# Optimization experiments

Hardware: AMD Instinct MI355X
Metric: run time of the kernel (lower is better)

## Reference

```python
import jax, jax.numpy as jnp
import numpy as np

E = 512
H = 8
D = E // H  # 64
B = 2
S = 4096


def setup_inputs() -> dict:
    key = jax.random.key(0)
    ks = jax.random.split(key, 12)
    s = 1.0 / np.sqrt(E)
    return {
        "x": jax.random.normal(ks[0], (B, S, E), dtype=jnp.float32),
        "bias": jax.random.normal(ks[1], (H, 1, S, S), dtype=jnp.float32),
        "mask": jax.random.randint(ks[2], (1, 1, S, S), 0, 2, dtype=jnp.int32),
        "Wq": jax.random.normal(ks[3], (E, E), dtype=jnp.float32) * s,
        "bq": jnp.zeros((E,), dtype=jnp.float32),
        "Wk": jax.random.normal(ks[4], (E, E), dtype=jnp.float32) * s,
        "bk": jnp.zeros((E,), dtype=jnp.float32),
        "Wv": jax.random.normal(ks[5], (E, E), dtype=jnp.float32) * s,
        "bv": jnp.zeros((E,), dtype=jnp.float32),
        "Wo": jax.random.normal(ks[6], (E, E), dtype=jnp.float32) * s,
        "bo": jnp.zeros((E,), dtype=jnp.float32),
    }


def _split_heads(t):
    # [B,S,E] -> [H,B,S,D]  (matches x.view(B,-1,H,D).permute(2,0,1,3))
    b, s, _ = t.shape
    return t.reshape(b, s, H, D).transpose(2, 0, 1, 3)


def reference(x, bias, mask, Wq, bq, Wk, bk, Wv, bv, Wo, bo):
    # torch Linear: y = x @ W.T + b
    q = _split_heads(x @ Wq.T + bq)  # [H,B,S,D]
    k = _split_heads(x @ Wk.T + bk)
    v = _split_heads(x @ Wv.T + bv)

    scores = jnp.einsum("hbqd,hbkd->hbqk", q, k) + bias  # [H,B,S,S]
    scores = jnp.where(mask == 0, jnp.float32(-1e20), scores)
    # NOTE: original divides AFTER bias-add and masking
    probs = jax.nn.softmax(scores / jnp.sqrt(jnp.float32(D)), axis=-1)
    out = jnp.einsum("hbqk,hbkd->hbqd", probs, v)  # [H,B,S,D]
    out = out.transpose(1, 2, 0, 3).reshape(x.shape[0], -1, H * D)  # [B,S,E]
    return out @ Wo.T + bo
```

## Files before the change

### kernel.cpp

```cpp
#include <hip/hip_runtime.h>
#include <hip/hip_bf16.h>

typedef __bf16 bf16x8 __attribute__((ext_vector_type(8)));
typedef float f32x4 __attribute__((ext_vector_type(4)));

#define S_LEN 4096
#define EMB   512
#define NHEAD 8
#define HDIM  64
#define NBAT  2
#define NROW  (NBAT * S_LEN)

static __device__ __forceinline__ f32x4 mfma16x16(bf16x8 a, bf16x8 b, f32x4 c) {
    return __builtin_amdgcn_mfma_f32_16x16x32_bf16(a, b, c, 0, 0, 0);
}

__global__ __launch_bounds__(256) void convert_kernel(
    const float* __restrict__ x, const float* __restrict__ Wq,
    const float* __restrict__ Wk, const float* __restrict__ Wv,
    const float* __restrict__ Wo,
    __hip_bfloat16* __restrict__ xb, __hip_bfloat16* __restrict__ wqkv,
    __hip_bfloat16* __restrict__ wob)
{
    const int NX = NROW * EMB;
    const int NW = EMB * EMB;
    int i = blockIdx.x * 256 + threadIdx.x;
    if (i < NX) { xb[i] = __float2bfloat16(x[i]); return; }
    int j = i - NX;
    if (j < 3 * NW) {
        int p = j >> 18, r = j & (NW - 1);
        const float* src = (p == 0) ? Wq : (p == 1) ? Wk : Wv;
        wqkv[j] = __float2bfloat16(src[r]);
    } else if (j < 4 * NW) {
        int r = j - 3 * NW;
        wob[r] = __float2bfloat16(Wo[r]);
    }
}

__device__ __forceinline__ void gemm_core(
    const __hip_bfloat16* __restrict__ A, const __hip_bfloat16* __restrict__ Bw,
    int mbase, int nbase,
    __hip_bfloat16* As, __hip_bfloat16* Bs, f32x4 acc[2][4])
{
    const int tid = threadIdx.x;
    const int w = tid >> 6, lane = tid & 63, l = lane & 15, quad = lane >> 4;
    const f32x4 zero = {0.f, 0.f, 0.f, 0.f};
#pragma unroll
    for (int mb = 0; mb < 2; mb++)
#pragma unroll
        for (int nb = 0; nb < 4; nb++) acc[mb][nb] = zero;

    for (int k0 = 0; k0 < EMB; k0 += 32) {
        __syncthreads();
#pragma unroll
        for (int c = tid; c < 512; c += 256) {
            int row = c >> 2, kc = c & 3;
            uint4 v = *(const uint4*)(A + (size_t)(mbase + row) * EMB + k0 + kc * 8);
            *(uint4*)(As + row * 40 + kc * 8) = v;
        }
        {
            int row = tid >> 2, kc = tid & 3;
            uint4 v = *(const uint4*)(Bw + (size_t)(nbase + row) * EMB + k0 + kc * 8);
            *(uint4*)(Bs + row * 40 + kc * 8) = v;
        }
        __syncthreads();

        bf16x8 af[2], bfr[4];
#pragma unroll
        for (int mb = 0; mb < 2; mb++)
            af[mb] = *(const bf16x8*)(As + (w * 32 + mb * 16 + l) * 40 + quad * 8);
#pragma unroll
        for (int nb = 0; nb < 4; nb++)
            bfr[nb] = *(const bf16x8*)(Bs + (nb * 16 + l) * 40 + quad * 8);
#pragma unroll
        for (int mb = 0; mb < 2; mb++)
#pragma unroll
            for (int nb = 0; nb < 4; nb++)
                acc[mb][nb] = mfma16x16(af[mb], bfr[nb], acc[mb][nb]);
    }
}

__global__ __launch_bounds__(256, 4) void qkv_gemm(
    const __hip_bfloat16* __restrict__ xb, const __hip_bfloat16* __restrict__ wqkv,
    const float* __restrict__ bq, const float* __restrict__ bk, const float* __restrict__ bv,
    __hip_bfloat16* __restrict__ Qh, __hip_bfloat16* __restrict__ Kh,
    __hip_bfloat16* __restrict__ Vt)
{
    __shared__ __align__(16) __hip_bfloat16 As[128 * 40];
    __shared__ __align__(16) __hip_bfloat16 Bs[64 * 40];
    const int mbase = blockIdx.x * 128, nbase = blockIdx.y * 64;
    f32x4 acc[2][4];
    gemm_core(xb, wqkv, mbase, nbase, As, Bs, acc);

    const int tid = threadIdx.x;
    const int w = tid >> 6, lane = tid & 63, l = lane & 15, quad = lane >> 4;
    const int p = nbase >> 9;
    const float* bias = (p == 0) ? bq : (p == 1) ? bk : bv;
    __hip_bfloat16* dst = (p == 0) ? Qh : (p == 1) ? Kh : Vt;
#pragma unroll
    for (int mb = 0; mb < 2; mb++)
#pragma unroll
        for (int nb = 0; nb < 4; nb++)
#pragma unroll
            for (int r = 0; r < 4; r++) {
                int m = mbase + w * 32 + mb * 16 + quad * 4 + r;
                int n = nbase + nb * 16 + l;
                int o = n & 511;
                float v = acc[mb][nb][r] + bias[o];
                int b = m >> 12, s = m & 4095, hh = o >> 6, d = o & 63;
                size_t idx = (p == 2)
                    ? ((size_t)((hh * 2 + b) * 64 + d)) * 4096 + s
                    : ((size_t)((hh * 2 + b) * 4096 + s)) * 64 + d;
                dst[idx] = __float2bfloat16(v);
            }
}

__global__ __launch_bounds__(256, 2) void attn_kernel(
    const __hip_bfloat16* __restrict__ Qh, const __hip_bfloat16* __restrict__ Kh,
    const __hip_bfloat16* __restrict__ Vt,
    const float* __restrict__ bias, const int* __restrict__ mask,
    __hip_bfloat16* __restrict__ Om)
{
    const int h = blockIdx.y, qt = blockIdx.x;
    const int tid = threadIdx.x;
    const int w = tid >> 6, lane = tid & 63, l = lane & 15, quad = lane >> 4;
    const int q0 = qt * 64;
    const float CS = 0.18033688011112042f;

    __shared__ __align__(16) __hip_bfloat16 Ks[2][64 * 72];
    __shared__ __align__(16) __hip_bfloat16 Vs[2][64 * 72];
    __shared__ __align__(16) __hip_bfloat16 Ps[64 * 72];

    bf16x8 qf[2][2];
#pragma unroll
    for (int b = 0; b < 2; b++) {
        const __hip_bfloat16* qp =
            Qh + ((size_t)((h * 2 + b) * 4096 + q0 + w * 16 + l)) * 64;
        qf[b][0] = *(const bf16x8*)(qp + quad * 8);
        qf[b][1] = *(const bf16x8*)(qp + 32 + quad * 8);
    }

    f32x4 oacc[2][4];
    float mst[2][4], lst[2][4];
    const f32x4 zero = {0.f, 0.f, 0.f, 0.f};
#pragma unroll
    for (int b = 0; b < 2; b++) {
#pragma unroll
        for (int nb = 0; nb < 4; nb++) oacc[b][nb] = zero;
#pragma unroll
        for (int r = 0; r < 4; r++) { mst[b][r] = -__builtin_inff(); lst[b][r] = 0.f; }
    }

    for (int kt = 0; kt < 64; kt++) {
        const int k0 = kt * 64;
        __syncthreads();
#pragma unroll
        for (int c = tid; c < 2048; c += 256) {
            int t = c >> 9;
            int b = t & 1, isV = t >> 1;
            int cc = c & 511, row = cc >> 3, ch = cc & 7;
            const __hip_bfloat16* src = isV
                ? Vt + ((size_t)((h * 2 + b) * 64 + row)) * 4096 + k0 + ch * 8
                : Kh + ((size_t)((h * 2 + b) * 4096 + k0 + row)) * 64 + ch * 8;
            uint4 v = *(const uint4*)src;
            *(uint4*)((isV ? Vs[b] : Ks[b]) + row * 72 + ch * 8) = v;
        }
        float bor[4][4];
#pragma unroll
        for (int nb = 0; nb < 4; nb++)
#pragma unroll
            for (int r = 0; r < 4; r++) {
                int qq = q0 + w * 16 + quad * 4 + r;
                int kk = k0 + nb * 16 + l;
                float bb = bias[(size_t)h * S_LEN * S_LEN + (size_t)qq * S_LEN + kk];
                int mm = mask[(size_t)qq * S_LEN + kk];
                bor[nb][r] = mm ? bb : -1e30f;
            }
        __syncthreads();

#pragma unroll
        for (int b = 0; b < 2; b++) {
            f32x4 sc[4] = {zero, zero, zero, zero};
#pragma unroll
            for (int ks = 0; ks < 2; ks++)
#pragma unroll
                for (int nb = 0; nb < 4; nb++) {
                    bf16x8 kf = *(const bf16x8*)(Ks[b] + (nb * 16 + l) * 72 + ks * 32 + quad * 8);
                    sc[nb] = mfma16x16(qf[b][ks], kf, sc[nb]);
                }
            float xv[4][4], rmax[4];
#pragma unroll
            for (int r = 0; r < 4; r++) rmax[r] = -__builtin_inff();
#pragma unroll
            for (int nb = 0; nb < 4; nb++)
#pragma unroll
                for (int r = 0; r < 4; r++) {
                    xv[nb][r] = (sc[nb][r] + bor[nb][r]) * CS;
                    rmax[r] = fmaxf(rmax[r], xv[nb][r]);
                }
#pragma unroll
            for (int r = 0; r < 4; r++) {
                rmax[r] = fmaxf(rmax[r], __shfl_xor(rmax[r], 1));
                rmax[r] = fmaxf(rmax[r], __shfl_xor(rmax[r], 2));
                rmax[r] = fmaxf(rmax[r], __shfl_xor(rmax[r], 4));
                rmax[r] = fmaxf(rmax[r], __shfl_xor(rmax[r], 8));
            }
            float alpha[4], rsum[4];
#pragma unroll
            for (int r = 0; r < 4; r++) {
                float mn = fmaxf(mst[b][r], rmax[r]);
                alpha[r] = __builtin_amdgcn_exp2f(mst[b][r] - mn);
                mst[b][r] = mn;
                rsum[r] = 0.f;
            }
            float pv[4][4];
#pragma unroll
            for (int nb = 0; nb < 4; nb++)
#pragma unroll
                for (int r = 0; r < 4; r++) {
                    float e = __builtin_amdgcn_exp2f(xv[nb][r] - mst[b][r]);
                    pv[nb][r] = e;
                    rsum[r] += e;
                }
#pragma unroll
            for (int r = 0; r < 4; r++) {
                rsum[r] += __shfl_xor(rsum[r], 1);
                rsum[r] += __shfl_xor(rsum[r], 2);
                rsum[r] += __shfl_xor(rsum[r], 4);
                rsum[r] += __shfl_xor(rsum[r], 8);
                lst[b][r] = lst[b][r] * alpha[r] + rsum[r];
            }
#pragma unroll
            for (int nb = 0; nb < 4; nb++)
#pragma unroll
                for (int r = 0; r < 4; r++) oacc[b][nb][r] *= alpha[r];
#pragma unroll
            for (int nb = 0; nb < 4; nb++)
#pragma unroll
                for (int r = 0; r < 4; r++)
                    Ps[(w * 16 + quad * 4 + r) * 72 + nb * 16 + l] =
                        __float2bfloat16(pv[nb][r]);
#pragma unroll
            for (int ks = 0; ks < 2; ks++) {
                bf16x8 pf = *(const bf16x8*)(Ps + (w * 16 + l) * 72 + ks * 32 + quad * 8);
#pragma unroll
                for (int nb = 0; nb < 4; nb++) {
                    bf16x8 vf = *(const bf16x8*)(Vs[b] + (nb * 16 + l) * 72 + ks * 32 + quad * 8);
                    oacc[b][nb] = mfma16x16(pf, vf, oacc[b][nb]);
                }
            }
        }
    }

#pragma unroll
    for (int b = 0; b < 2; b++)
#pragma unroll
        for (int nb = 0; nb < 4; nb++)
#pragma unroll
            for (int r = 0; r < 4; r++) {
                int qq = q0 + w * 16 + quad * 4 + r;
                float val = oacc[b][nb][r] / lst[b][r];
                Om[((size_t)(b * 4096 + qq)) * 512 + h * 64 + nb * 16 + l] =
                    __float2bfloat16(val);
            }
}

__global__ __launch_bounds__(256, 4) void out_gemm(
    const __hip_bfloat16* __restrict__ Om, const __hip_bfloat16* __restrict__ wob,
    const float* __restrict__ bo, float* __restrict__ out)
{
    __shared__ __align__(16) __hip_bfloat16 As[128 * 40];
    __shared__ __align__(16) __hip_bfloat16 Bs[64 * 40];
    const int mbase = blockIdx.x * 128, nbase = blockIdx.y * 64;
    f32x4 acc[2][4];
    gemm_core(Om, wob, mbase, nbase, As, Bs, acc);

    const int tid = threadIdx.x;
    const int w = tid >> 6, lane = tid & 63, l = lane & 15, quad = lane >> 4;
#pragma unroll
    for (int mb = 0; mb < 2; mb++)
#pragma unroll
        for (int nb = 0; nb < 4; nb++)
#pragma unroll
            for (int r = 0; r < 4; r++) {
                int m = mbase + w * 32 + mb * 16 + quad * 4 + r;
                int n = nbase + nb * 16 + l;
                out[(size_t)m * EMB + n] = acc[mb][nb][r] + bo[n];
            }
}

extern "C" void kernel_launch(void* const* d_in, const int* in_sizes, int n_in,
                              void* d_out, int out_size, void* d_ws, size_t ws_size,
                              hipStream_t stream) {
    const float* x    = (const float*)d_in[0];
    const float* bias = (const float*)d_in[1];
    const int*   mask = (const int*)d_in[2];
    const float* Wq   = (const float*)d_in[3];
    const float* bq   = (const float*)d_in[4];
    const float* Wk   = (const float*)d_in[5];
    const float* bk   = (const float*)d_in[6];
    const float* Wv   = (const float*)d_in[7];
    const float* bv   = (const float*)d_in[8];
    const float* Wo   = (const float*)d_in[9];
    const float* bo   = (const float*)d_in[10];
    float* out = (float*)d_out;

    char* ws = (char*)d_ws;
    __hip_bfloat16* xb   = (__hip_bfloat16*)ws; ws += (size_t)NROW * EMB * 2;
    __hip_bfloat16* wqkv = (__hip_bfloat16*)ws; ws += (size_t)3 * EMB * EMB * 2;
    __hip_bfloat16* wob  = (__hip_bfloat16*)ws; ws += (size_t)EMB * EMB * 2;
    __hip_bfloat16* Qh   = (__hip_bfloat16*)ws; ws += (size_t)NROW * EMB * 2;
    __hip_bfloat16* Kh   = (__hip_bfloat16*)ws; ws += (size_t)NROW * EMB * 2;
    __hip_bfloat16* Vt   = (__hip_bfloat16*)ws; ws += (size_t)NROW * EMB * 2;
    __hip_bfloat16* Om   = (__hip_bfloat16*)ws; ws += (size_t)NROW * EMB * 2;

    convert_kernel<<<dim3(20480), dim3(256), 0, stream>>>(
        x, Wq, Wk, Wv, Wo, xb, wqkv, wob);
    qkv_gemm<<<dim3(64, 24), dim3(256), 0, stream>>>(
        xb, wqkv, bq, bk, bv, Qh, Kh, Vt);
    attn_kernel<<<dim3(64, NHEAD), dim3(256), 0, stream>>>(
        Qh, Kh, Vt, bias, mask, Om);
    out_gemm<<<dim3(64, 8), dim3(256), 0, stream>>>(Om, wob, bo, out);
}
```

Baseline: 1.321 ms.

## Prefetch K/V and bias/mask into registers, split batches across waves, add V transpose kernel

The attention kernel now prefetches the next tile's K/V, bias and mask into registers while computing the current tile. Each wave handles one batch instead of both, so each block covers 32 queries and the grid doubles to 128x8 with a higher occupancy hint. The V transpose moves out of scattered qkv_gemm stores into a separate LDS-based transpose kernel that reuses the xb buffer. The aim is to hide global-load latency and improve store coalescing, at the cost of more registers per thread, one extra launch, and loading each K/V tile for half as many queries.

```diff
diff --git a/kernel.cpp b/kernel.cpp
--- a/kernel.cpp
+++ b/kernel.cpp
@@ -84,7 +84,7 @@
     const __hip_bfloat16* __restrict__ xb, const __hip_bfloat16* __restrict__ wqkv,
     const float* __restrict__ bq, const float* __restrict__ bk, const float* __restrict__ bv,
     __hip_bfloat16* __restrict__ Qh, __hip_bfloat16* __restrict__ Kh,
-    __hip_bfloat16* __restrict__ Vt)
+    __hip_bfloat16* __restrict__ Vh)
 {
     __shared__ __align__(16) __hip_bfloat16 As[128 * 40];
     __shared__ __align__(16) __hip_bfloat16 Bs[64 * 40];
@@ -96,7 +96,7 @@
     const int w = tid >> 6, lane = tid & 63, l = lane & 15, quad = lane >> 4;
     const int p = nbase >> 9;
     const float* bias = (p == 0) ? bq : (p == 1) ? bk : bv;
-    __hip_bfloat16* dst = (p == 0) ? Qh : (p == 1) ? Kh : Vt;
+    __hip_bfloat16* dst = (p == 0) ? Qh : (p == 1) ? Kh : Vh;
 #pragma unroll
     for (int mb = 0; mb < 2; mb++)
 #pragma unroll
@@ -108,14 +108,35 @@
                 int o = n & 511;
                 float v = acc[mb][nb][r] + bias[o];
                 int b = m >> 12, s = m & 4095, hh = o >> 6, d = o & 63;
-                size_t idx = (p == 2)
-                    ? ((size_t)((hh * 2 + b) * 64 + d)) * 4096 + s
-                    : ((size_t)((hh * 2 + b) * 4096 + s)) * 64 + d;
-                dst[idx] = __float2bfloat16(v);
-            }
-}
-
-__global__ __launch_bounds__(256, 2) void attn_kernel(
+                dst[((size_t)((hh * 2 + b) * 4096 + s)) * 64 + d] = __float2bfloat16(v);
+            }
+}
+
+__global__ __launch_bounds__(256) void vtrans(
+    const __hip_bfloat16* __restrict__ Vh, __hip_bfloat16* __restrict__ Vt)
+{
+    __shared__ __align__(16) __hip_bfloat16 T[64 * 72];
+    const int st = blockIdx.x, hb = blockIdx.y, tid = threadIdx.x;
+    const int s0 = st * 64;
+    const __hip_bfloat16* src = Vh + ((size_t)hb * 4096 + s0) * 64;
+#pragma unroll
+    for (int i = 0; i < 2; i++) {
+        int c = tid + 256 * i, row = c >> 3, ch = c & 7;
+        uint4 v = *(const uint4*)(src + row * 64 + ch * 8);
+        *(uint4*)(T + row * 72 + ch * 8) = v;
+    }
+    __syncthreads();
+#pragma unroll
+    for (int i = 0; i < 2; i++) {
+        int c = tid + 256 * i, d = c >> 3, ch = c & 7;
+        __hip_bfloat16 tmp[8];
+#pragma unroll
+        for (int j = 0; j < 8; j++) tmp[j] = T[(ch * 8 + j) * 72 + d];
+        *(uint4*)(Vt + ((size_t)(hb * 64 + d)) * 4096 + s0 + ch * 8) = *(uint4*)tmp;
+    }
+}
+
+__global__ __launch_bounds__(256, 3) void attn_kernel(
     const __hip_bfloat16* __restrict__ Qh, const __hip_bfloat16* __restrict__ Kh,
     const __hip_bfloat16* __restrict__ Vt,
     const float* __restrict__ bias, const int* __restrict__ mask,
@@ -124,145 +145,163 @@
     const int h = blockIdx.y, qt = blockIdx.x;
     const int tid = threadIdx.x;
     const int w = tid >> 6, lane = tid & 63, l = lane & 15, quad = lane >> 4;
-    const int q0 = qt * 64;
+    const int bw = w & 1, wq = w >> 1;
+    const int qr = qt * 32 + wq * 16;
     const float CS = 0.18033688011112042f;
 
     __shared__ __align__(16) __hip_bfloat16 Ks[2][64 * 72];
     __shared__ __align__(16) __hip_bfloat16 Vs[2][64 * 72];
-    __shared__ __align__(16) __hip_bfloat16 Ps[64 * 72];
-
-    bf16x8 qf[2][2];
-#pragma unroll
-    for (int b = 0; b < 2; b++) {
-        const __hip_bfloat16* qp =
-            Qh + ((size_t)((h * 2 + b) * 4096 + q0 + w * 16 + l)) * 64;
-        qf[b][0] = *(const bf16x8*)(qp + quad * 8);
-        qf[b][1] = *(const bf16x8*)(qp + 32 + quad * 8);
-    }
-
-    f32x4 oacc[2][4];
-    float mst[2][4], lst[2][4];
+    __shared__ __align__(16) __hip_bfloat16 Ps[4][16 * 72];
+    __hip_bfloat16* ps = Ps[w];
+
+    const __hip_bfloat16* qp = Qh + ((size_t)((h * 2 + bw) * 4096 + qr + l)) * 64;
+    bf16x8 qf0 = *(const bf16x8*)(qp + quad * 8);
+    bf16x8 qf1 = *(const bf16x8*)(qp + 32 + quad * 8);
+
+    const float* bptr = bias + (size_t)h * S_LEN * S_LEN;
+
+    f32x4 oacc[4];
+    float mst[4], lst[4];
     const f32x4 zero = {0.f, 0.f, 0.f, 0.f};
 #pragma unroll
-    for (int b = 0; b < 2; b++) {
-#pragma unroll
-        for (int nb = 0; nb < 4; nb++) oacc[b][nb] = zero;
-#pragma unroll
-        for (int r = 0; r < 4; r++) { mst[b][r] = -__builtin_inff(); lst[b][r] = 0.f; }
-    }
-
-    for (int kt = 0; kt < 64; kt++) {
-        const int k0 = kt * 64;
-        __syncthreads();
-#pragma unroll
-        for (int c = tid; c < 2048; c += 256) {
-            int t = c >> 9;
-            int b = t & 1, isV = t >> 1;
-            int cc = c & 511, row = cc >> 3, ch = cc & 7;
+    for (int nb = 0; nb < 4; nb++) oacc[nb] = zero;
+#pragma unroll
+    for (int r = 0; r < 4; r++) { mst[r] = -__builtin_inff(); lst[r] = 0.f; }
+
+    uint4 kvbuf[8];
+    float bbuf[4][4];
+    int   mbuf[4][4];
+
+    auto kv_load = [&](int k0) {
+#pragma unroll
+        for (int i = 0; i < 8; i++) {
+            int c = tid + 256 * i;
+            int b = (c >> 9) & 1, isV = c >> 10;
+            int row = (c >> 3) & 63, ch = c & 7;
             const __hip_bfloat16* src = isV
                 ? Vt + ((size_t)((h * 2 + b) * 64 + row)) * 4096 + k0 + ch * 8
                 : Kh + ((size_t)((h * 2 + b) * 4096 + k0 + row)) * 64 + ch * 8;
-            uint4 v = *(const uint4*)src;
-            *(uint4*)((isV ? Vs[b] : Ks[b]) + row * 72 + ch * 8) = v;
-        }
+            kvbuf[i] = *(const uint4*)src;
+        }
+    };
+    auto bm_load = [&](int k0) {
+#pragma unroll
+        for (int nb = 0; nb < 4; nb++)
+#pragma unroll
+            for (int r = 0; r < 4; r++) {
+                size_t off = (size_t)(qr + quad * 4 + r) * S_LEN + k0 + nb * 16 + l;
+                bbuf[nb][r] = bptr[off];
+                mbuf[nb][r] = mask[off];
+            }
+    };
+
+    kv_load(0);
+    bm_load(0);
+
+    for (int kt = 0; kt < 64; kt++) {
+        __syncthreads();
+#pragma unroll
+        for (int i = 0; i < 8; i++) {
+            int c = tid + 256 * i;
+            int b = (c >> 9) & 1, isV = c >> 10;
+            int row = (c >> 3) & 63, ch = c & 7;
+            *(uint4*)((isV ? Vs[b] : Ks[b]) + row * 72 + ch * 8) = kvbuf[i];
+        }
+        __syncthreads();
+
         float bor[4][4];
 #pragma unroll
         for (int nb = 0; nb < 4; nb++)
 #pragma unroll
-            for (int r = 0; r < 4; r++) {
-                int qq = q0 + w * 16 + quad * 4 + r;
-                int kk = k0 + nb * 16 + l;
-                float bb = bias[(size_t)h * S_LEN * S_LEN + (size_t)qq * S_LEN + kk];
-                int mm = mask[(size_t)qq * S_LEN + kk];
-                bor[nb][r] = mm ? bb : -1e30f;
-            }
-        __syncthreads();
-
-#pragma unroll
-        for (int b = 0; b < 2; b++) {
-            f32x4 sc[4] = {zero, zero, zero, zero};
-#pragma unroll
-            for (int ks = 0; ks < 2; ks++)
-#pragma unroll
-                for (int nb = 0; nb < 4; nb++) {
-                    bf16x8 kf = *(const bf16x8*)(Ks[b] + (nb * 16 + l) * 72 + ks * 32 + quad * 8);
-                    sc[nb] = mfma16x16(qf[b][ks], kf, sc[nb]);
-                }
-            float xv[4][4], rmax[4];
-#pragma unroll
-            for (int r = 0; r < 4; r++) rmax[r] = -__builtin_inff();
-#pragma unroll
-            for (int nb = 0; nb < 4; nb++)
-#pragma unroll
-                for (int r = 0; r < 4; r++) {
-                    xv[nb][r] = (sc[nb][r] + bor[nb][r]) * CS;
-                    rmax[r] = fmaxf(rmax[r], xv[nb][r]);
-                }
-#pragma unroll
-            for (int r = 0; r < 4; r++) {
-                rmax[r] = fmaxf(rmax[r], __shfl_xor(rmax[r], 1));
-                rmax[r] = fmaxf(rmax[r], __shfl_xor(rmax[r], 2));
-                rmax[r] = fmaxf(rmax[r], __shfl_xor(rmax[r], 4));
-                rmax[r] = fmaxf(rmax[r], __shfl_xor(rmax[r], 8));
-            }
-            float alpha[4], rsum[4];
-#pragma unroll
-            for (int r = 0; r < 4; r++) {
-                float mn = fmaxf(mst[b][r], rmax[r]);
-                alpha[r] = __builtin_amdgcn_exp2f(mst[b][r] - mn);
-                mst[b][r] = mn;
-                rsum[r] = 0.f;
-            }
-            float pv[4][4];
-#pragma unroll
-            for (int nb = 0; nb < 4; nb++)
-#pragma unroll
-                for (int r = 0; r < 4; r++) {
-                    float e = __builtin_amdgcn_exp2f(xv[nb][r] - mst[b][r]);
-                    pv[nb][r] = e;
-                    rsum[r] += e;
-                }
-#pragma unroll
-            for (int r = 0; r < 4; r++) {
-                rsum[r] += __shfl_xor(rsum[r], 1);
-                rsum[r] += __shfl_xor(rsum[r], 2);
-                rsum[r] += __shfl_xor(rsum[r], 4);
-                rsum[r] += __shfl_xor(rsum[r], 8);
-                lst[b][r] = lst[b][r] * alpha[r] + rsum[r];
-            }
-#pragma unroll
-            for (int nb = 0; nb < 4; nb++)
-#pragma unroll
-                for (int r = 0; r < 4; r++) oacc[b][nb][r] *= alpha[r];
-#pragma unroll
-            for (int nb = 0; nb < 4; nb++)
-#pragma unroll
-                for (int r = 0; r < 4; r++)
-                    Ps[(w * 16 + quad * 4 + r) * 72 + nb * 16 + l] =
-                        __float2bfloat16(pv[nb][r]);
-#pragma unroll
-            for (int ks = 0; ks < 2; ks++) {
-                bf16x8 pf = *(const bf16x8*)(Ps + (w * 16 + l) * 72 + ks * 32 + quad * 8);
-#pragma unroll
-                for (int nb = 0; nb < 4; nb++) {
-                    bf16x8 vf = *(const bf16x8*)(Vs[b] + (nb * 16 + l) * 72 + ks * 32 + quad * 8);
-                    oacc[b][nb] = mfma16x16(pf, vf, oacc[b][nb]);
-                }
-            }
-        }
-    }
-
-#pragma unroll
-    for (int b = 0; b < 2; b++)
-#pragma unroll
-        for (int nb = 0; nb < 4; nb++)
-#pragma unroll
-            for (int r = 0; r < 4; r++) {
-                int qq = q0 + w * 16 + quad * 4 + r;
-                float val = oacc[b][nb][r] / lst[b][r];
-                Om[((size_t)(b * 4096 + qq)) * 512 + h * 64 + nb * 16 + l] =
-                    __float2bfloat16(val);
-            }
+            for (int r = 0; r < 4; r++)
+                bor[nb][r] = mbuf[nb][r] ? bbuf[nb][r] : -1e30f;
+
+        int k0n = (kt < 63) ? (kt + 1) * 64 : kt * 64;
+        kv_load(k0n);
+        bm_load(k0n);
+
+        f32x4 sc[4] = {zero, zero, zero, zero};
+#pragma unroll
+        for (int nb = 0; nb < 4; nb++) {
+            bf16x8 kf0 = *(const bf16x8*)(Ks[bw] + (nb * 16 + l) * 72 + quad * 8);
+            bf16x8 kf1 = *(const bf16x8*)(Ks[bw] + (nb * 16 + l) * 72 + 32 + quad * 8);
+            sc[nb] = mfma16x16(qf0, kf0, sc[nb]);
+            sc[nb] = mfma16x16(qf1, kf1, sc[nb]);
+        }
+
+        float xv[4][4], rmax[4];
+#pragma unroll
+        for (int r = 0; r < 4; r++) rmax[r] = -__builtin_inff();
+#pragma unroll
+        for (int nb = 0; nb < 4; nb++)
+#pragma unroll
+            for (int r = 0; r < 4; r++) {
+                xv[nb][r] = (sc[nb][r] + bor[nb][r]) * CS;
+                rmax[r] = fmaxf(rmax[r], xv[nb][r]);
+            }
+#pragma unroll
+        for (int r = 0; r < 4; r++) {
+            rmax[r] = fmaxf(rmax[r], __shfl_xor(rmax[r], 1));
+            rmax[r] = fmaxf(rmax[r], __shfl_xor(rmax[r], 2));
+            rmax[r] = fmaxf(rmax[r], __shfl_xor(rmax[r], 4));
+            rmax[r] = fmaxf(rmax[r], __shfl_xor(rmax[r], 8));
+        }
+        float alpha[4], rsum[4];
+#pragma unroll
+        for (int r = 0; r < 4; r++) {
+            float mn = fmaxf(mst[r], rmax[r]);
+            alpha[r] = __builtin_amdgcn_exp2f(mst[r] - mn);
+            mst[r] = mn;
+            rsum[r] = 0.f;
+        }
+        float pv[4][4];
+#pragma unroll
+        for (int nb = 0; nb < 4; nb++)
+#pragma unroll
+            for (int r = 0; r < 4; r++) {
+                float e = __builtin_amdgcn_exp2f(xv[nb][r] - mst[r]);
+                pv[nb][r] = e;
+                rsum[r] += e;
+            }
+#pragma unroll
+        for (int r = 0; r < 4; r++) {
+            rsum[r] += __shfl_xor(rsum[r], 1);
+            rsum[r] += __shfl_xor(rsum[r], 2);
+            rsum[r] += __shfl_xor(rsum[r], 4);
+            rsum[r] += __shfl_xor(rsum[r], 8);
+            lst[r] = lst[r] * alpha[r] + rsum[r];
+        }
+#pragma unroll
+        for (int nb = 0; nb < 4; nb++)
+#pragma unroll
+            for (int r = 0; r < 4; r++) oacc[nb][r] *= alpha[r];
+
+#pragma unroll
+        for (int nb = 0; nb < 4; nb++)
+#pragma unroll
+            for (int r = 0; r < 4; r++)
+                ps[(quad * 4 + r) * 72 + nb * 16 + l] = __float2bfloat16(pv[nb][r]);
+
+#pragma unroll
+        for (int ks = 0; ks < 2; ks++) {
+            bf16x8 pf = *(const bf16x8*)(ps + l * 72 + ks * 32 + quad * 8);
+#pragma unroll
+            for (int nb = 0; nb < 4; nb++) {
+                bf16x8 vf = *(const bf16x8*)(Vs[bw] + (nb * 16 + l) * 72 + ks * 32 + quad * 8);
+                oacc[nb] = mfma16x16(pf, vf, oacc[nb]);
+            }
+        }
+    }
+
+#pragma unroll
+    for (int nb = 0; nb < 4; nb++)
+#pragma unroll
+        for (int r = 0; r < 4; r++) {
+            int qq = qr + quad * 4 + r;
+            float val = oacc[nb][r] / lst[r];
+            Om[((size_t)(bw * 4096 + qq)) * 512 + h * 64 + nb * 16 + l] =
+                __float2bfloat16(val);
+        }
 }
 
 __global__ __launch_bounds__(256, 4) void out_gemm(
@@ -311,14 +350,16 @@
     __hip_bfloat16* wob  = (__hip_bfloat16*)ws; ws += (size_t)EMB * EMB * 2;
     __hip_bfloat16* Qh   = (__hip_bfloat16*)ws; ws += (size_t)NROW * EMB * 2;
     __hip_bfloat16* Kh   = (__hip_bfloat16*)ws; ws += (size_t)NROW * EMB * 2;
-    __hip_bfloat16* Vt   = (__hip_bfloat16*)ws; ws += (size_t)NROW * EMB * 2;
+    __hip_bfloat16* Vh   = (__hip_bfloat16*)ws; ws += (size_t)NROW * EMB * 2;
     __hip_bfloat16* Om   = (__hip_bfloat16*)ws; ws += (size_t)NROW * EMB * 2;
+    __hip_bfloat16* Vt   = xb;
 
     convert_kernel<<<dim3(20480), dim3(256), 0, stream>>>(
         x, Wq, Wk, Wv, Wo, xb, wqkv, wob);
     qkv_gemm<<<dim3(64, 24), dim3(256), 0, stream>>>(
-        xb, wqkv, bq, bk, bv, Qh, Kh, Vt);
-    attn_kernel<<<dim3(64, NHEAD), dim3(256), 0, stream>>>(
+        xb, wqkv, bq, bk, bv, Qh, Kh, Vh);
+    vtrans<<<dim3(64, 16), dim3(256), 0, stream>>>(Vh, Vt);
+    attn_kernel<<<dim3(128, NHEAD), dim3(256), 0, stream>>>(
         Qh, Kh, Vt, bias, mask, Om);
     out_gemm<<<dim3(64, 8), dim3(256), 0, stream>>>(Om, wob, bo, out);
 }
```

Measured after the change: 1.579 ms. +19.5%, slower.
